# Kernel tuning notes

Measured on AMD Instinct MI355X. Metric: run time of the kernel, lower is better.

The kernel has to match this reference:

```python
import jax, jax.numpy as jnp
import numpy as np

B, T, D, H = 4, 4096, 2048, 128

def setup_inputs() -> dict:
    key = jax.random.key(0)
    k1, k2, k3, k4 = jax.random.split(key, 4)
    scale = 0.02
    return {
        "x": jax.random.normal(k1, (B, T, D), dtype=jnp.float32),
        "Wq": jax.random.normal(k2, (D, H), dtype=jnp.float32) * scale,
        "Wk": jax.random.normal(k3, (D, H), dtype=jnp.float32) * scale,
        "Wv": jax.random.normal(k4, (D, H), dtype=jnp.float32) * scale,
    }

def reference(x, Wq, Wk, Wv):
    # x: [B,T,D]; projections to [B,T,H]
    q = jnp.einsum('btd,dh->bth', x, Wq)
    k = jnp.einsum('btd,dh->bth', x, Wk)
    v = jnp.einsum('btd,dh->bth', x, Wv)
    scale = 1.0 / jnp.sqrt(jnp.asarray(q.shape[-1], q.dtype))
    scores = jnp.einsum('bth,bsh->bts', q, k) * scale  # [B,T,T]
    t = x.shape[1]
    causal = jnp.tril(jnp.ones((t, t), dtype=bool))
    scores = jnp.where(causal, scores, -jnp.inf)
    weights = jax.nn.softmax(scores, axis=-1)
    # dropout p=0.0 (eval) -> identity
    out = jnp.einsum('bts,bsh->bth', weights, v)
    return out
```

## Files before the change

kernel.cpp:

```cpp
#include <hip/hip_runtime.h>
#include <hip/hip_bf16.h>

#define Bq 4
#define Tq 4096
#define Dq 2048
#define Hq 128
#define Mq (Bq*Tq)
#define CHUNK 16

typedef __attribute__((ext_vector_type(8))) short bf16x8;
typedef __attribute__((ext_vector_type(4))) float f32x4;

static __device__ __forceinline__ short bfbits(float f) {
    union { __hip_bfloat16 h; short s; } u;
    u.h = __float2bfloat16(f);
    return u.s;
}
static __device__ __forceinline__ float bf2f(short s) {
    union { unsigned u; float f; } v;
    v.u = ((unsigned)(unsigned short)s) << 16;
    return v.f;
}
#define WAIT_LDS() __builtin_amdgcn_s_waitcnt(0xC07F)

static __device__ __forceinline__ void gload16(const void* g, void* l) {
    __builtin_amdgcn_global_load_lds(
        (const __attribute__((address_space(1))) unsigned int*)g,
        (__attribute__((address_space(3))) unsigned int*)l, 16, 0, 0);
}

__global__ __launch_bounds__(256, 1) void wt_kernel(
    const float* __restrict__ Wqp,
    const float* __restrict__ Wkp,
    const float* __restrict__ Wvp,
    short* __restrict__ wTg)
{
    __shared__ short trsp[128][136];
    const int kc = blockIdx.x;
    const int w  = blockIdx.y;
    const float* __restrict__ W = (w == 0) ? Wqp : (w == 1) ? Wkp : Wvp;
    const float scale = (w == 0) ? 0.08838834764831843f : 1.0f;
    const int t = threadIdx.x;

    #pragma unroll
    for (int i = 0; i < 16; i++) {
        int idx = t + i * 256;
        int r = idx >> 5, c4 = idx & 31;
        float4 f = *(const float4*)&W[(size_t)(kc * 128 + r) * Hq + c4 * 4];
        trsp[c4 * 4 + 0][r] = bfbits(f.x * scale);
        trsp[c4 * 4 + 1][r] = bfbits(f.y * scale);
        trsp[c4 * 4 + 2][r] = bfbits(f.z * scale);
        trsp[c4 * 4 + 3][r] = bfbits(f.w * scale);
    }
    __syncthreads();
    #pragma unroll
    for (int i = 0; i < 8; i++) {
        int idx = t + i * 256;
        int h = idx >> 4, c8 = idx & 15;
        *(bf16x8*)&wTg[((size_t)w * 128 + h) * Dq + kc * 128 + c8 * 8] =
            *(bf16x8*)&trsp[h][c8 * 8];
    }
}

__global__ __launch_bounds__(512, 4) void qkv_fused_kernel(
    const float* __restrict__ x,
    const short* __restrict__ wTg,
    short* __restrict__ qg,
    short* __restrict__ kg,
    short* __restrict__ vTt)
{
    __shared__ __attribute__((aligned(128))) char smem[53248];

    const int m0   = blockIdx.x * 32;
    const int t    = threadIdx.x;
    const int l    = t & 63;
    const int w    = t >> 6;
    const int l15  = l & 15;
    const int quad = l >> 4;
    const int wn   = w * 48;

    f32x4 o[2][3];
    #pragma unroll
    for (int mf = 0; mf < 2; mf++)
        #pragma unroll
        for (int j = 0; j < 3; j++) o[mf][j] = (f32x4){0.f, 0.f, 0.f, 0.f};

    const short* wsrc = wTg + (size_t)(w * 48 + (l >> 2)) * Dq + (l & 3) * 8;
    const int xrow = t >> 4;
    const float* xsrc = x + (size_t)(m0 + xrow) * Dq + (t & 15) * 2;

    float2 xr0, xr1;

    #define ISSUE_W(it2, buf)                                                    \
        do {                                                                     \
            char* wb_ = smem + (buf) * 26624 + 2048;                             \
            _Pragma("unroll")                                                    \
            for (int j = 0; j < 3; j++)                                          \
                gload16(wsrc + (size_t)j * 16 * Dq + (it2) * 32,                 \
                        wb_ + (w * 3 + j) * 1024);                               \
        } while (0)

    #define WRITE_X(buf, xr)                                                     \
        do {                                                                     \
            char* xb_ = smem + (buf) * 26624;                                    \
            unsigned pk = (unsigned)(unsigned short)bfbits(xr.x)                 \
                        | ((unsigned)(unsigned short)bfbits(xr.y) << 16);        \
            *(unsigned*)(xb_ + xrow * 64 + (t & 15) * 4) = pk;                   \
        } while (0)

    #define COMPUTE(par)                                                         \
        do {                                                                     \
            const char* xb_ = smem + (par) * 26624;                              \
            const char* wb_ = xb_ + 2048;                                        \
            bf16x8 a0 = *(const bf16x8*)(xb_ + (l15)      * 64 + quad * 16);     \
            bf16x8 a1 = *(const bf16x8*)(xb_ + (16 + l15) * 64 + quad * 16);     \
            bf16x8 b0 = *(const bf16x8*)(wb_ + (wn +      l15) * 64 + quad * 16);\
            bf16x8 b1 = *(const bf16x8*)(wb_ + (wn + 16 + l15) * 64 + quad * 16);\
            bf16x8 b2 = *(const bf16x8*)(wb_ + (wn + 32 + l15) * 64 + quad * 16);\
            o[0][0] = __builtin_amdgcn_mfma_f32_16x16x32_bf16(a0, b0, o[0][0], 0, 0, 0); \
            o[1][0] = __builtin_amdgcn_mfma_f32_16x16x32_bf16(a1, b0, o[1][0], 0, 0, 0); \
            o[0][1] = __builtin_amdgcn_mfma_f32_16x16x32_bf16(a0, b1, o[0][1], 0, 0, 0); \
            o[1][1] = __builtin_amdgcn_mfma_f32_16x16x32_bf16(a1, b1, o[1][1], 0, 0, 0); \
            o[0][2] = __builtin_amdgcn_mfma_f32_16x16x32_bf16(a0, b2, o[0][2], 0, 0, 0); \
            o[1][2] = __builtin_amdgcn_mfma_f32_16x16x32_bf16(a1, b2, o[1][2], 0, 0, 0); \
        } while (0)

    #define BODY(it, par, xrNew, xrOld)                                          \
        do {                                                                     \
            __builtin_amdgcn_s_barrier();                                        \
            __builtin_amdgcn_sched_barrier(0);                                   \
            COMPUTE(par);                                                        \
            __builtin_amdgcn_s_barrier();                                        \
            __builtin_amdgcn_sched_barrier(0);                                   \
            ISSUE_W((it) + 2, par);                                              \
            xrNew = *(const float2*)(xsrc + ((it) + 2) * 32);                    \
            asm volatile("s_waitcnt vmcnt(4)" ::: "memory");                     \
            WRITE_X(1 - (par), xrOld);                                           \
            asm volatile("s_waitcnt lgkmcnt(0)" ::: "memory");                   \
            __builtin_amdgcn_sched_barrier(0);                                   \
        } while (0)

    ISSUE_W(0, 0);
    xr0 = *(const float2*)(xsrc + 0);
    ISSUE_W(1, 1);
    xr1 = *(const float2*)(xsrc + 32);
    asm volatile("s_waitcnt vmcnt(3)" ::: "memory");
    WRITE_X(0, xr0);
    asm volatile("s_waitcnt lgkmcnt(0)" ::: "memory");
    __builtin_amdgcn_sched_barrier(0);

    #pragma unroll 1
    for (int itp = 0; itp < 31; itp++) {
        const int it = itp * 2;
        BODY(it,     0, xr0, xr1);
        BODY(it + 1, 1, xr1, xr0);
    }
    __builtin_amdgcn_s_barrier();
    __builtin_amdgcn_sched_barrier(0);
    COMPUTE(0);
    __builtin_amdgcn_s_barrier();
    __builtin_amdgcn_sched_barrier(0);
    asm volatile("s_waitcnt vmcnt(0)" ::: "memory");
    WRITE_X(1, xr1);
    asm volatile("s_waitcnt lgkmcnt(0)" ::: "memory");
    __builtin_amdgcn_sched_barrier(0);
    __builtin_amdgcn_s_barrier();
    COMPUTE(1);
    __builtin_amdgcn_s_barrier();

    #undef BODY
    #undef COMPUTE
    #undef WRITE_X
    #undef ISSUE_W

    {
        short (*e64)[264] = (short(*)[264])smem;
        #pragma unroll
        for (int mf = 0; mf < 2; mf++)
            #pragma unroll
            for (int j = 0; j < 3; j++) {
                int n0 = wn + j * 16;
                if (n0 < 256) {
                    #pragma unroll
                    for (int reg = 0; reg < 4; reg++)
                        e64[mf * 16 + quad * 4 + reg][n0 + l15] = bfbits(o[mf][j][reg]);
                }
            }
        __syncthreads();
        #pragma unroll
        for (int i = 0; i < 2; i++) {
            int idx = t + i * 512;
            int r = idx >> 5, u = idx & 31;
            int n = u * 8;
            bf16x8 val = *(bf16x8*)&e64[r][n];
            short* dst = (n < 128) ? &qg[(size_t)(m0 + r) * Hq + n]
                                   : &kg[(size_t)(m0 + r) * Hq + (n - 128)];
            *(bf16x8*)dst = val;
        }
    }
    __syncthreads();
    {
        short (*e128)[40] = (short(*)[40])smem;
        #pragma unroll
        for (int mf = 0; mf < 2; mf++)
            #pragma unroll
            for (int j = 0; j < 3; j++) {
                int n0 = wn + j * 16;
                if (n0 >= 256) {
                    short4 pk;
                    pk.x = bfbits(o[mf][j][0]); pk.y = bfbits(o[mf][j][1]);
                    pk.z = bfbits(o[mf][j][2]); pk.w = bfbits(o[mf][j][3]);
                    *(short4*)&e128[(n0 - 256) + l15][mf * 16 + quad * 4] = pk;
                }
            }
        __syncthreads();
        const int bb   = m0 / Tq;
        const int jt   = (m0 % Tq) >> 6;
        const int moff = m0 & 63;
        {
            int h = t >> 2, u = t & 3;
            *(bf16x8*)&vTt[(((size_t)bb * (Tq / 64) + jt) * 128 + h) * 64 + moff + u * 8] =
                *(bf16x8*)&e128[h][u * 8];
        }
    }
}

__global__ __launch_bounds__(256, 3) void attn_part_kernel(
    const short* __restrict__ qg, const short* __restrict__ kg,
    const short* __restrict__ vTt,
    short* __restrict__ Opart,
    float* __restrict__ lv)
{
    __shared__ short ks_s[64][136];
    __shared__ short vt_s[128][72];
    __shared__ short ps_s[64][72];

    const int qt = blockIdx.x;
    const int b  = blockIdx.y;
    const int c  = blockIdx.z;
    const int q0 = qt * 64;

    const int lo = c * CHUNK;
    const int hi = min(qt + 1, lo + CHUNK);
    if (lo >= hi) return;

    const int t    = threadIdx.x;
    const int lane = t & 63;
    const int qw   = t >> 6;
    const int l15  = lane & 15;
    const int quad = lane >> 4;

    bf16x8 qf[4];
    {
        const short* qsrc = qg + (size_t)(b * Tq + q0 + qw * 16 + l15) * Hq + quad * 8;
        #pragma unroll
        for (int kk = 0; kk < 4; kk++)
            qf[kk] = *(const bf16x8*)(qsrc + kk * 32);
    }

    float lsum[4] = {0.f, 0.f, 0.f, 0.f};
    f32x4 o[8];
    #pragma unroll
    for (int nf = 0; nf < 8; nf++) o[nf] = (f32x4){0.f, 0.f, 0.f, 0.f};

    bf16x8 kreg[4], vreg[4];
    {
        const size_t kbase = (size_t)(b * Tq + lo * 64) * Hq;
        const short* vsrc = vTt + (((size_t)b * (Tq / 64) + lo) * 128) * 64;
        #pragma unroll
        for (int i = 0; i < 4; i++) {
            int idx = t + i * 256;
            kreg[i] = *(const bf16x8*)&kg[kbase + (size_t)(idx >> 4) * Hq + (idx & 15) * 8];
            vreg[i] = *(const bf16x8*)&vsrc[idx * 8];
        }
        #pragma unroll
        for (int i = 0; i < 4; i++) {
            int idx = t + i * 256;
            *(bf16x8*)&ks_s[idx >> 4][(idx & 15) * 8] = kreg[i];
            *(bf16x8*)&vt_s[idx >> 3][(idx & 7) * 8]  = vreg[i];
        }
    }
    __syncthreads();

    for (int jt = lo; jt < hi; jt++) {
        if (jt + 1 < hi) {
            const size_t kbase = (size_t)(b * Tq + (jt + 1) * 64) * Hq;
            const short* vsrc = vTt + (((size_t)b * (Tq / 64) + jt + 1) * 128) * 64;
            #pragma unroll
            for (int i = 0; i < 4; i++) {
                int idx = t + i * 256;
                kreg[i] = *(const bf16x8*)&kg[kbase + (size_t)(idx >> 4) * Hq + (idx & 15) * 8];
                vreg[i] = *(const bf16x8*)&vsrc[idx * 8];
            }
        }

        f32x4 sacc[4];
        #pragma unroll
        for (int nf = 0; nf < 4; nf++) sacc[nf] = (f32x4){0.f, 0.f, 0.f, 0.f};
        #pragma unroll
        for (int kk = 0; kk < 4; kk++) {
            bf16x8 bk[4];
            #pragma unroll
            for (int nf = 0; nf < 4; nf++)
                bk[nf] = *(bf16x8*)&ks_s[nf * 16 + l15][kk * 32 + quad * 8];
            #pragma unroll
            for (int nf = 0; nf < 4; nf++)
                sacc[nf] = __builtin_amdgcn_mfma_f32_16x16x32_bf16(qf[kk], bk[nf], sacc[nf], 0, 0, 0);
        }

        const bool diag = (jt == qt);
        #pragma unroll
        for (int reg = 0; reg < 4; reg++) {
            const int rloc = qw * 16 + quad * 4 + reg;
            #pragma unroll
            for (int nf = 0; nf < 4; nf++) {
                float s = sacc[nf][reg];
                if (diag && (nf * 16 + l15 > rloc)) s = -1e30f;
                float p = __expf(s);
                lsum[reg] += p;
                ps_s[rloc][nf * 16 + l15] = bfbits(p);
            }
        }
        WAIT_LDS();

        #pragma unroll
        for (int ks2 = 0; ks2 < 2; ks2++) {
            bf16x8 ap = *(bf16x8*)&ps_s[qw * 16 + l15][ks2 * 32 + quad * 8];
            bf16x8 bv[8];
            #pragma unroll
            for (int nf = 0; nf < 8; nf++)
                bv[nf] = *(bf16x8*)&vt_s[nf * 16 + l15][ks2 * 32 + quad * 8];
            #pragma unroll
            for (int nf = 0; nf < 8; nf++)
                o[nf] = __builtin_amdgcn_mfma_f32_16x16x32_bf16(ap, bv[nf], o[nf], 0, 0, 0);
        }

        __syncthreads();
        if (jt + 1 < hi) {
            #pragma unroll
            for (int i = 0; i < 4; i++) {
                int idx = t + i * 256;
                *(bf16x8*)&ks_s[idx >> 4][(idx & 15) * 8] = kreg[i];
                *(bf16x8*)&vt_s[idx >> 3][(idx & 7) * 8]  = vreg[i];
            }
            __syncthreads();
        }
    }

    #pragma unroll
    for (int reg = 0; reg < 4; reg++) {
        #pragma unroll
        for (int mm = 8; mm >= 1; mm >>= 1)
            lsum[reg] += __shfl_xor(lsum[reg], mm, 16);
    }
    const size_t zoff = (size_t)c * Mq;
    if (l15 == 0) {
        #pragma unroll
        for (int reg = 0; reg < 4; reg++)
            lv[zoff + (size_t)b * Tq + q0 + qw * 16 + quad * 4 + reg] = lsum[reg];
    }

    __syncthreads();
    short (*epi)[136] = (short(*)[136])&ks_s[0][0];
    #pragma unroll
    for (int nf = 0; nf < 8; nf++)
        #pragma unroll
        for (int reg = 0; reg < 4; reg++)
            epi[qw * 16 + quad * 4 + reg][nf * 16 + l15] = bfbits(o[nf][reg]);
    __syncthreads();
    #pragma unroll
    for (int i = 0; i < 4; i++) {
        int idx = t + i * 256;
        int r = idx >> 4, cc = idx & 15;
        *(bf16x8*)&Opart[(zoff + (size_t)b * Tq + q0 + r) * Hq + cc * 8] =
            *(bf16x8*)&epi[r][cc * 8];
    }
}

__global__ __launch_bounds__(256, 4) void merge_kernel(
    const short* __restrict__ Opart, const float* __restrict__ lv,
    float* __restrict__ outg)
{
    const int t   = threadIdx.x;
    const int row = blockIdx.x * 16 + (t >> 4);
    const int cu  = t & 15;

    const int rl  = row & (Tq - 1);
    const int nch = (rl >> 10) + 1;

    float lsum = 0.f;
    float acc[8] = {};
    for (int cc = 0; cc < nch; cc++) {
        lsum += lv[(size_t)cc * Mq + row];
        bf16x8 oc = *(const bf16x8*)&Opart[((size_t)cc * Mq + row) * Hq + cu * 8];
        #pragma unroll
        for (int j = 0; j < 8; j++) acc[j] += bf2f(oc[j]);
    }
    float inv = 1.0f / lsum;

    float4 r0, r1;
    r0.x = acc[0] * inv; r0.y = acc[1] * inv; r0.z = acc[2] * inv; r0.w = acc[3] * inv;
    r1.x = acc[4] * inv; r1.y = acc[5] * inv; r1.z = acc[6] * inv; r1.w = acc[7] * inv;
    float* dst = &outg[(size_t)row * Hq + cu * 8];
    *(float4*)dst       = r0;
    *(float4*)(dst + 4) = r1;
}

extern "C" void kernel_launch(void* const* d_in, const int* in_sizes, int n_in,
                              void* d_out, int out_size, void* d_ws, size_t ws_size,
                              hipStream_t stream) {
    const float* x   = (const float*)d_in[0];
    const float* Wqp = (const float*)d_in[1];
    const float* Wkp = (const float*)d_in[2];
    const float* Wvp = (const float*)d_in[3];
    float* out = (float*)d_out;

    short* qg    = (short*)d_ws;
    short* kg    = qg  + (size_t)Mq * Hq;
    short* vTt   = kg  + (size_t)Mq * Hq;
    short* Opart = vTt + (size_t)Mq * Hq;
    short* wTg   = Opart;
    float* lv    = (float*)(Opart + (size_t)4 * Mq * Hq);

    wt_kernel<<<dim3(16, 3), dim3(256), 0, stream>>>(Wqp, Wkp, Wvp, wTg);
    qkv_fused_kernel<<<dim3(Mq / 32), dim3(512), 0, stream>>>(x, wTg, qg, kg, vTt);
    attn_part_kernel<<<dim3(Tq / 64, Bq, 4), dim3(256), 0, stream>>>(qg, kg, vTt, Opart, lv);
    merge_kernel<<<dim3(Mq / 16), dim3(256), 0, stream>>>(Opart, lv, out);
}
```

Baseline: 313.6 us.

## Enlarge QKV projection tile to 64 rows and 64-wide K with swizzled LDS

Doubles the QKV projection block tile from 32 to 64 rows and the K step from 32 to 64, so each loaded weight tile is reused across twice as many rows and the main loop runs half as many iterations and barriers. LDS layouts for x and W gain an XOR swizzle to avoid bank conflicts with the 128-byte row stride. x loads are widened to float4 pairs and issued earlier in the iteration. The cost is more LDS and accumulator registers per block, which lowers occupancy from 4 to 2 blocks per CU and halves the grid size.

```diff
diff --git a/kernel.cpp b/kernel.cpp
--- a/kernel.cpp
+++ b/kernel.cpp
@@ -20,6 +20,10 @@
     union { unsigned u; float f; } v;
     v.u = ((unsigned)(unsigned short)s) << 16;
     return v.f;
+}
+static __device__ __forceinline__ unsigned pk2(float a, float b) {
+    return ((unsigned)(unsigned short)bfbits(a)) |
+           (((unsigned)(unsigned short)bfbits(b)) << 16);
 }
 #define WAIT_LDS() __builtin_amdgcn_s_waitcnt(0xC07F)
 
@@ -62,121 +66,144 @@
     }
 }
 
-__global__ __launch_bounds__(512, 4) void qkv_fused_kernel(
+__global__ __launch_bounds__(512, 2) void qkv_fused_kernel(
     const float* __restrict__ x,
     const short* __restrict__ wTg,
     short* __restrict__ qg,
     short* __restrict__ kg,
     short* __restrict__ vTt)
 {
-    __shared__ __attribute__((aligned(128))) char smem[53248];
-
-    const int m0   = blockIdx.x * 32;
+    __shared__ __attribute__((aligned(128))) char smem[114688];
+
+    const int m0   = blockIdx.x * 64;
     const int t    = threadIdx.x;
     const int l    = t & 63;
     const int w    = t >> 6;
     const int l15  = l & 15;
     const int quad = l >> 4;
     const int wn   = w * 48;
-
-    f32x4 o[2][3];
-    #pragma unroll
-    for (int mf = 0; mf < 2; mf++)
+    const int swz  = (l15 & 7) << 4;
+
+    f32x4 o[4][3];
+    #pragma unroll
+    for (int mf = 0; mf < 4; mf++)
         #pragma unroll
         for (int j = 0; j < 3; j++) o[mf][j] = (f32x4){0.f, 0.f, 0.f, 0.f};
 
-    const short* wsrc = wTg + (size_t)(w * 48 + (l >> 2)) * Dq + (l & 3) * 8;
-    const int xrow = t >> 4;
-    const float* xsrc = x + (size_t)(m0 + xrow) * Dq + (t & 15) * 2;
-
-    float2 xr0, xr1;
-
-    #define ISSUE_W(it2, buf)                                                    \
+    const short* wsrc = wTg + (size_t)(w * 48 + (l >> 3)) * Dq
+                            + (((l & 7) ^ (l >> 3)) << 3);
+    const int xr = t >> 3;
+    const float* xsrc = x + (size_t)(m0 + xr) * Dq + (t & 7) * 8;
+    const int xwb = xr * 128 + (((t & 7) ^ (xr & 7)) << 4);
+
+    float4 xg[2][2];
+
+    #define ISSUE_W(it2, par)                                                    \
         do {                                                                     \
-            char* wb_ = smem + (buf) * 26624 + 2048;                             \
+            char* wb_ = smem + 16384 + (par) * 49152;                            \
             _Pragma("unroll")                                                    \
-            for (int j = 0; j < 3; j++)                                          \
-                gload16(wsrc + (size_t)j * 16 * Dq + (it2) * 32,                 \
-                        wb_ + (w * 3 + j) * 1024);                               \
+            for (int j = 0; j < 6; j++)                                          \
+                gload16(wsrc + (size_t)j * 8 * Dq + (it2) * 64,                  \
+                        wb_ + (w * 6 + j) * 1024);                               \
         } while (0)
 
-    #define WRITE_X(buf, xr)                                                     \
+    #define LOAD_X(it2, s)                                                       \
         do {                                                                     \
-            char* xb_ = smem + (buf) * 26624;                                    \
-            unsigned pk = (unsigned)(unsigned short)bfbits(xr.x)                 \
-                        | ((unsigned)(unsigned short)bfbits(xr.y) << 16);        \
-            *(unsigned*)(xb_ + xrow * 64 + (t & 15) * 4) = pk;                   \
+            xg[s][0] = *(const float4*)(xsrc + (it2) * 64);                      \
+            xg[s][1] = *(const float4*)(xsrc + (it2) * 64 + 4);                  \
+        } while (0)
+
+    #define WRITE_X(par, s)                                                      \
+        do {                                                                     \
+            uint4 px;                                                            \
+            px.x = pk2(xg[s][0].x, xg[s][0].y);                                  \
+            px.y = pk2(xg[s][0].z, xg[s][0].w);                                  \
+            px.z = pk2(xg[s][1].x, xg[s][1].y);                                  \
+            px.w = pk2(xg[s][1].z, xg[s][1].w);                                  \
+            *(uint4*)(smem + (par) * 8192 + xwb) = px;                           \
         } while (0)
 
     #define COMPUTE(par)                                                         \
         do {                                                                     \
-            const char* xb_ = smem + (par) * 26624;                              \
-            const char* wb_ = xb_ + 2048;                                        \
-            bf16x8 a0 = *(const bf16x8*)(xb_ + (l15)      * 64 + quad * 16);     \
-            bf16x8 a1 = *(const bf16x8*)(xb_ + (16 + l15) * 64 + quad * 16);     \
-            bf16x8 b0 = *(const bf16x8*)(wb_ + (wn +      l15) * 64 + quad * 16);\
-            bf16x8 b1 = *(const bf16x8*)(wb_ + (wn + 16 + l15) * 64 + quad * 16);\
-            bf16x8 b2 = *(const bf16x8*)(wb_ + (wn + 32 + l15) * 64 + quad * 16);\
-            o[0][0] = __builtin_amdgcn_mfma_f32_16x16x32_bf16(a0, b0, o[0][0], 0, 0, 0); \
-            o[1][0] = __builtin_amdgcn_mfma_f32_16x16x32_bf16(a1, b0, o[1][0], 0, 0, 0); \
-            o[0][1] = __builtin_amdgcn_mfma_f32_16x16x32_bf16(a0, b1, o[0][1], 0, 0, 0); \
-            o[1][1] = __builtin_amdgcn_mfma_f32_16x16x32_bf16(a1, b1, o[1][1], 0, 0, 0); \
-            o[0][2] = __builtin_amdgcn_mfma_f32_16x16x32_bf16(a0, b2, o[0][2], 0, 0, 0); \
-            o[1][2] = __builtin_amdgcn_mfma_f32_16x16x32_bf16(a1, b2, o[1][2], 0, 0, 0); \
+            const char* xb_ = smem + (par) * 8192;                               \
+            const char* wb_ = smem + 16384 + (par) * 49152;                      \
+            _Pragma("unroll")                                                    \
+            for (int kk = 0; kk < 2; kk++) {                                     \
+                const int kb_ = kk * 64 + quad * 16;                             \
+                bf16x8 a[4], b[3];                                               \
+                _Pragma("unroll")                                                \
+                for (int mf = 0; mf < 4; mf++)                                   \
+                    a[mf] = *(const bf16x8*)(xb_ + (mf * 16 + l15) * 128         \
+                                                 + (kb_ ^ swz));                 \
+                _Pragma("unroll")                                                \
+                for (int j = 0; j < 3; j++)                                      \
+                    b[j] = *(const bf16x8*)(wb_ + (wn + j * 16 + l15) * 128      \
+                                                + (kb_ ^ swz));                  \
+                _Pragma("unroll")                                                \
+                for (int mf = 0; mf < 4; mf++)                                   \
+                    _Pragma("unroll")                                            \
+                    for (int j = 0; j < 3; j++)                                  \
+                        o[mf][j] = __builtin_amdgcn_mfma_f32_16x16x32_bf16(      \
+                            a[mf], b[j], o[mf][j], 0, 0, 0);                     \
+            }                                                                    \
         } while (0)
 
-    #define BODY(it, par, xrNew, xrOld)                                          \
+    #define BODY(it, par)                                                        \
         do {                                                                     \
             __builtin_amdgcn_s_barrier();                                        \
+            asm volatile("s_waitcnt vmcnt(8)" ::: "memory");                     \
             __builtin_amdgcn_sched_barrier(0);                                   \
+            LOAD_X((it) + 2, par);                                               \
             COMPUTE(par);                                                        \
             __builtin_amdgcn_s_barrier();                                        \
+            ISSUE_W((it) + 2, par);                                              \
+            asm volatile("s_waitcnt vmcnt(8)" ::: "memory");                     \
             __builtin_amdgcn_sched_barrier(0);                                   \
-            ISSUE_W((it) + 2, par);                                              \
-            xrNew = *(const float2*)(xsrc + ((it) + 2) * 32);                    \
-            asm volatile("s_waitcnt vmcnt(4)" ::: "memory");                     \
-            WRITE_X(1 - (par), xrOld);                                           \
+            WRITE_X(1 - (par), 1 - (par));                                       \
             asm volatile("s_waitcnt lgkmcnt(0)" ::: "memory");                   \
             __builtin_amdgcn_sched_barrier(0);                                   \
         } while (0)
 
     ISSUE_W(0, 0);
-    xr0 = *(const float2*)(xsrc + 0);
+    LOAD_X(0, 0);
     ISSUE_W(1, 1);
-    xr1 = *(const float2*)(xsrc + 32);
-    asm volatile("s_waitcnt vmcnt(3)" ::: "memory");
-    WRITE_X(0, xr0);
+    asm volatile("s_waitcnt vmcnt(6)" ::: "memory");
+    __builtin_amdgcn_sched_barrier(0);
+    WRITE_X(0, 0);
+    LOAD_X(1, 1);
     asm volatile("s_waitcnt lgkmcnt(0)" ::: "memory");
     __builtin_amdgcn_sched_barrier(0);
 
     #pragma unroll 1
-    for (int itp = 0; itp < 31; itp++) {
+    for (int itp = 0; itp < 15; itp++) {
         const int it = itp * 2;
-        BODY(it,     0, xr0, xr1);
-        BODY(it + 1, 1, xr1, xr0);
+        BODY(it,     0);
+        BODY(it + 1, 1);
     }
     __builtin_amdgcn_s_barrier();
-    __builtin_amdgcn_sched_barrier(0);
     COMPUTE(0);
     __builtin_amdgcn_s_barrier();
+    asm volatile("s_waitcnt vmcnt(6)" ::: "memory");
     __builtin_amdgcn_sched_barrier(0);
-    asm volatile("s_waitcnt vmcnt(0)" ::: "memory");
-    WRITE_X(1, xr1);
+    WRITE_X(1, 1);
     asm volatile("s_waitcnt lgkmcnt(0)" ::: "memory");
     __builtin_amdgcn_sched_barrier(0);
     __builtin_amdgcn_s_barrier();
+    asm volatile("s_waitcnt vmcnt(0)" ::: "memory");
+    __builtin_amdgcn_sched_barrier(0);
     COMPUTE(1);
     __builtin_amdgcn_s_barrier();
 
     #undef BODY
     #undef COMPUTE
     #undef WRITE_X
+    #undef LOAD_X
     #undef ISSUE_W
 
     {
         short (*e64)[264] = (short(*)[264])smem;
         #pragma unroll
-        for (int mf = 0; mf < 2; mf++)
+        for (int mf = 0; mf < 4; mf++)
             #pragma unroll
             for (int j = 0; j < 3; j++) {
                 int n0 = wn + j * 16;
@@ -188,7 +215,7 @@
             }
         __syncthreads();
         #pragma unroll
-        for (int i = 0; i < 2; i++) {
+        for (int i = 0; i < 4; i++) {
             int idx = t + i * 512;
             int r = idx >> 5, u = idx & 31;
             int n = u * 8;
@@ -200,9 +227,9 @@
     }
     __syncthreads();
     {
-        short (*e128)[40] = (short(*)[40])smem;
-        #pragma unroll
-        for (int mf = 0; mf < 2; mf++)
+        short (*e128)[72] = (short(*)[72])smem;
+        #pragma unroll
+        for (int mf = 0; mf < 4; mf++)
             #pragma unroll
             for (int j = 0; j < 3; j++) {
                 int n0 = wn + j * 16;
@@ -214,12 +241,13 @@
                 }
             }
         __syncthreads();
-        const int bb   = m0 / Tq;
-        const int jt   = (m0 % Tq) >> 6;
-        const int moff = m0 & 63;
-        {
-            int h = t >> 2, u = t & 3;
-            *(bf16x8*)&vTt[(((size_t)bb * (Tq / 64) + jt) * 128 + h) * 64 + moff + u * 8] =
+        const int bb = m0 / Tq;
+        const int jt = (m0 % Tq) >> 6;
+        #pragma unroll
+        for (int i = 0; i < 2; i++) {
+            int idx = t + i * 512;
+            int h = idx >> 3, u = idx & 7;
+            *(bf16x8*)&vTt[(((size_t)bb * (Tq / 64) + jt) * 128 + h) * 64 + u * 8] =
                 *(bf16x8*)&e128[h][u * 8];
         }
     }
@@ -423,7 +451,7 @@
     float* lv    = (float*)(Opart + (size_t)4 * Mq * Hq);
 
     wt_kernel<<<dim3(16, 3), dim3(256), 0, stream>>>(Wqp, Wkp, Wvp, wTg);
-    qkv_fused_kernel<<<dim3(Mq / 32), dim3(512), 0, stream>>>(x, wTg, qg, kg, vTt);
+    qkv_fused_kernel<<<dim3(Mq / 64), dim3(512), 0, stream>>>(x, wTg, qg, kg, vTt);
     attn_part_kernel<<<dim3(Tq / 64, Bq, 4), dim3(256), 0, stream>>>(qg, kg, vTt, Opart, lv);
     merge_kernel<<<dim3(Mq / 16), dim3(256), 0, stream>>>(Opart, lv, out);
 }
```

Measured after the change: 275.2 us. 12.2% less time.
